# Kernel optimization log

Measured on AMD Instinct MI355X. Metric: run time of the kernel, lower is better.

Reference implementation:

```python
import jax, jax.numpy as jnp
import numpy as np

N = 100_000
E = 1_600_000
IN, HID, HEADS, OUT = 128, 64, 4, 64
LAYER_DIMS = [(IN, HEADS, HID // HEADS), (HID, HEADS, HID // HEADS), (HID, 1, OUT)]
NEG_SLOPE = 0.2


def setup_inputs() -> dict:
    key = jax.random.key(0)
    ks = jax.random.split(key, 20)
    inp = {}
    inp["x"] = jax.random.normal(ks[0], (N, IN), dtype=jnp.float32)
    # edges with src != dst by construction (module removes self loops, then adds them)
    for i in range(3):
        src = jax.random.randint(ks[1 + 2 * i], (E,), 0, N, dtype=jnp.int32)
        off = jax.random.randint(ks[2 + 2 * i], (E,), 1, N, dtype=jnp.int32)
        dst = ((src + off) % N).astype(jnp.int32)
        inp[f"edge_index{i}"] = jnp.stack([src, dst])
    k = 7
    for i, (cin, h, c) in enumerate(LAYER_DIMS):
        ws = 1.0 / np.sqrt(cin)
        inp[f"Wl{i}"] = jax.random.normal(ks[k], (cin, h * c), dtype=jnp.float32) * ws; k += 1
        inp[f"bl{i}"] = jnp.zeros((h * c,), dtype=jnp.float32)
        inp[f"Wr{i}"] = jax.random.normal(ks[k], (cin, h * c), dtype=jnp.float32) * ws; k += 1
        inp[f"br{i}"] = jnp.zeros((h * c,), dtype=jnp.float32)
        inp[f"att{i}"] = jax.random.normal(ks[k], (h, c), dtype=jnp.float32) * (1.0 / np.sqrt(c)); k += 1
        inp[f"bias{i}"] = jnp.zeros((h * c,), dtype=jnp.float32)
    return inp


def _l1norm(x):
    return x / jnp.maximum(jnp.sum(jnp.abs(x), axis=1, keepdims=True), 1e-12)


def _gat2conv(x, ei, Wl, bl, Wr, br, att, bias, heads, out_c):
    n = x.shape[0]
    xl = (x @ Wl + bl).reshape(n, heads, out_c)  # source-side features (x_j)
    xr = (x @ Wr + br).reshape(n, heads, out_c)  # target-side features (x_i)
    src, dst = ei[0], ei[1]
    s = jax.nn.leaky_relu(xl[src] + xr[dst], NEG_SLOPE)      # [E', H, C]
    a = jnp.einsum('ehc,hc->eh', s, att)                      # [E', H]
    m = jax.ops.segment_max(a, dst, num_segments=n)           # segment softmax over edges per target
    e = jnp.exp(a - m[dst])
    den = jax.ops.segment_sum(e, dst, num_segments=n)
    alpha = e / (den[dst] + 1e-16)
    msg = (xl[src] * alpha[:, :, None]).reshape(-1, heads * out_c)
    return jax.ops.segment_sum(msg, dst, num_segments=n) + bias  # concat heads + bias


def _forward(x, eis, params):
    loop = jnp.arange(N, dtype=eis[0].dtype)
    self_loops = jnp.stack([loop, loop])
    num_layers = len(LAYER_DIMS)
    for i, ((cin, h, c), p) in enumerate(zip(LAYER_DIMS, params)):
        ei = jnp.concatenate([eis[i], self_loops], axis=1)  # add_self_loops
        new_x = _gat2conv(x, ei, *p, h, c)
        x = new_x
        if i != num_layers - 1:
            x = jax.nn.relu(new_x)
        x = _l1norm(x)  # F.normalize(x, p=1)
    x = x / jnp.maximum(jnp.linalg.norm(x, axis=1, keepdims=True), 1e-12)  # F.normalize (L2)
    return jax.nn.relu(x)


def reference(x, edge_index0, edge_index1, edge_index2,
              Wl0, bl0, Wr0, br0, att0, bias0,
              Wl1, bl1, Wr1, br1, att1, bias1,
              Wl2, bl2, Wr2, br2, att2, bias2):
    eis = (edge_index0, edge_index1, edge_index2)
    params = [(Wl0, bl0, Wr0, br0, att0, bias0),
              (Wl1, bl1, Wr1, br1, att1, bias1),
              (Wl2, bl2, Wr2, br2, att2, bias2)]
    return _forward(x, eis, params)
```

## Files before the change

### kernel.cpp

```cpp
#include <hip/hip_runtime.h>
#include <hip/hip_fp16.h>
#include <string.h>

#define NN 100000
#define EE 1600000
#define CAP 64
#define NBIN 196
#define BINSZ 512
#define BINCAP 10400
#define CHA 2048
#define NCA 782
#define GGX 391

typedef __fp16 h2v __attribute__((ext_vector_type(2)));
typedef __fp16 half8 __attribute__((ext_vector_type(8)));
typedef float  f32x4 __attribute__((ext_vector_type(4)));

template<int CTRL>
__device__ __forceinline__ float dppadd(float x){
    int y = __builtin_amdgcn_update_dpp(0, __float_as_int(x), CTRL, 0xF, 0xF, true);
    return x + __int_as_float(y);
}
template<int H>
__device__ __forceinline__ float head_reduce32(float p){
    p = dppadd<0xB1>(p);
    p = dppadd<0x4E>(p);
    p = dppadd<0x141>(p);
    if constexpr (H == 1){
        p = dppadd<0x140>(p);
        p += __shfl_xor(p, 16);
    }
    return p;
}
__device__ __forceinline__ float red32(float p){
    p = dppadd<0xB1>(p);
    p = dppadd<0x4E>(p);
    p = dppadd<0x141>(p);
    p = dppadd<0x140>(p);
    p += __shfl_xor(p, 16);
    return p;
}


__global__ __launch_bounds__(256) void k_A(
    const int* __restrict__ e0, const int* __restrict__ e1, const int* __restrict__ e2,
    int* __restrict__ p0, int* __restrict__ p1, int* __restrict__ p2,
    int* __restrict__ tail)
{
    __shared__ int h4[4][NBIN];
    __shared__ int shist[NBIN], lbase[NBIN], gbase[NBIN], cur[NBIN];
    __shared__ int pk[CHA], spp[CHA];
    const int l = blockIdx.x / NCA, c = blockIdx.x % NCA;
    const int* ei = (l==0? e0 : l==1? e1 : e2);
    int* pr = (l==0? p0 : l==1? p1 : p2);
    const int base = c*CHA, n = min(CHA, EE-base);
    const int tid = threadIdx.x;
    const int wave = tid >> 6;
    for (int i=tid;i<4*NBIN;i+=256) ((int*)h4)[i]=0;
    __syncthreads();
    int dreg[CHA/256], sreg[CHA/256];
    #pragma unroll
    for (int j = 0; j < CHA/256; ++j){
        const int i = tid + j*256;
        if (i < n){ dreg[j] = ei[EE+base+i]; sreg[j] = ei[base+i]; }
        else { dreg[j] = -1; }
    }
    #pragma unroll
    for (int j = 0; j < CHA/256; ++j)
        if (dreg[j] >= 0) atomicAdd(&h4[wave][dreg[j]>>9],1);
    __syncthreads();
    for (int i=tid;i<NBIN;i+=256) shist[i] = h4[0][i]+h4[1][i]+h4[2][i]+h4[3][i];
    __syncthreads();
    if (tid==0){ int acc=0; for (int i=0;i<NBIN;++i){ lbase[i]=acc; acc+=shist[i]; } }
    __syncthreads();
    if (tid<NBIN){ gbase[tid] = atomicAdd(&tail[l*NBIN+tid], shist[tid]); cur[tid]=lbase[tid]; }
    __syncthreads();
    #pragma unroll
    for (int j = 0; j < CHA/256; ++j){
        if (dreg[j] < 0) continue;
        const int d = dreg[j], s = sreg[j];
        const int bb = d>>9;
        const int r = atomicAdd(&cur[bb],1);
        const int off = gbase[bb] + (r - lbase[bb]);
        pk[r] = (s << 9) | (d & 511);
        spp[r] = (off < BINCAP) ? (bb*BINCAP + off) : -1;
    }
    __syncthreads();
    for (int i=tid;i<n;i+=256){ const int p = spp[i]; if (p >= 0) pr[p] = pk[i]; }
}

__global__ __launch_bounds__(256) void k_B(
    const int* __restrict__ p0, const int* __restrict__ p1, const int* __restrict__ p2,
    const int* __restrict__ tail,
    int* __restrict__ c0, int* __restrict__ s0,
    int* __restrict__ c1, int* __restrict__ s1,
    int* __restrict__ c2, int* __restrict__ s2)
{
    __shared__ int cnt[BINSZ];
    __shared__ __align__(16) int sl[BINSZ*CAP];
    const int l = blockIdx.x / NBIN, b = blockIdx.x % NBIN;
    const int* pr = (l==0? p0 : l==1? p1 : p2) + (size_t)b*BINCAP;
    int* gc = (l==0? c0 : l==1? c1 : c2);
    int* gs = (l==0? s0 : l==1? s1 : s2);
    const int n0 = b*BINSZ;
    const int nn = min(BINSZ, NN - n0);
    const int tid = threadIdx.x;
    for (int i=tid;i<nn;i+=256){ cnt[i]=1; sl[i*CAP]= n0+i; }
    __syncthreads();
    const int ec = min(tail[l*NBIN+b], BINCAP);
    for (int i=tid;i<ec;i+=256){
        const int pv = pr[i];
        const int nd = pv & 511;
        const int p = atomicAdd(&cnt[nd],1);
        if (p < CAP) sl[nd*CAP+p] = pv >> 9;
    }
    __syncthreads();
    for (int i=tid;i<nn;i+=256) gc[n0+i] = cnt[i];
    const int t4 = nn*(CAP/4);
    int4* gs4 = (int4*)(gs + (size_t)n0*CAP);
    const int4* sl4 = (const int4*)sl;
    for (int i=tid;i<t4;i+=256) gs4[i] = sl4[i];
}


template<int CIN>
__global__ __launch_bounds__(256) void k_gemm(
    const float* __restrict__ x,
    const float* __restrict__ Wl, const float* __restrict__ bl,
    const float* __restrict__ Wr, const float* __restrict__ br,
    __half* __restrict__ xlh, float* __restrict__ xr)
{
    constexpr int KC = CIN / 32;
    const int tid = threadIdx.x;
    const int wave = tid >> 6, lane = tid & 63;
    const int m = lane & 15, g = lane >> 4;
    const int side = blockIdx.y;
    const float* __restrict__ W  = side ? Wr : Wl;
    const float* __restrict__ bb = side ? br : bl;

    half8 bf[4][KC];
    #pragma unroll
    for (int ct = 0; ct < 4; ++ct)
        #pragma unroll
        for (int kc = 0; kc < KC; ++kc)
            #pragma unroll
            for (int i = 0; i < 8; ++i)
                bf[ct][kc][i] = (__fp16)W[(kc*32 + g*8 + i)*64 + ct*16 + m];

    float bv[4];
    #pragma unroll
    for (int ct = 0; ct < 4; ++ct) bv[ct] = bb[ct*16 + m];

    const int stride = GGX * 64;
    for (int row0 = blockIdx.x*64 + wave*16; row0 < NN; row0 += stride){
        half8 a[KC];
        const float* xp = x + (size_t)(row0 + m) * CIN + g*8;
        #pragma unroll
        for (int kc = 0; kc < KC; ++kc){
            const float4 u = *(const float4*)(xp + kc*32);
            const float4 v = *(const float4*)(xp + kc*32 + 4);
            a[kc][0]=(__fp16)u.x; a[kc][1]=(__fp16)u.y; a[kc][2]=(__fp16)u.z; a[kc][3]=(__fp16)u.w;
            a[kc][4]=(__fp16)v.x; a[kc][5]=(__fp16)v.y; a[kc][6]=(__fp16)v.z; a[kc][7]=(__fp16)v.w;
        }
        f32x4 acc0 = {0,0,0,0}, acc1 = {0,0,0,0}, acc2 = {0,0,0,0}, acc3 = {0,0,0,0};
        #pragma unroll
        for (int kc = 0; kc < KC; ++kc){
            acc0 = __builtin_amdgcn_mfma_f32_16x16x32_f16(a[kc], bf[0][kc], acc0, 0,0,0);
            acc1 = __builtin_amdgcn_mfma_f32_16x16x32_f16(a[kc], bf[1][kc], acc1, 0,0,0);
            acc2 = __builtin_amdgcn_mfma_f32_16x16x32_f16(a[kc], bf[2][kc], acc2, 0,0,0);
            acc3 = __builtin_amdgcn_mfma_f32_16x16x32_f16(a[kc], bf[3][kc], acc3, 0,0,0);
        }
        #pragma unroll
        for (int j = 0; j < 4; ++j){
            const size_t rb = (size_t)(row0 + 4*g + j)*64 + m;
            const float o0 = acc0[j] + bv[0];
            const float o1 = acc1[j] + bv[1];
            const float o2 = acc2[j] + bv[2];
            const float o3 = acc3[j] + bv[3];
            if (side){
                xr[rb]    = o0; xr[rb+16] = o1; xr[rb+32] = o2; xr[rb+48] = o3;
            } else {
                xlh[rb]    = __float2half_rn(o0);
                xlh[rb+16] = __float2half_rn(o1);
                xlh[rb+32] = __float2half_rn(o2);
                xlh[rb+48] = __float2half_rn(o3);
            }
        }
    }
}

template<int H, bool LAST>
__global__ __launch_bounds__(256) void k_fused(
    const int* __restrict__ cnt, const int* __restrict__ slots,
    const __half* __restrict__ xlh, const float* __restrict__ xr,
    const float* __restrict__ att, const float* __restrict__ bias,
    float* __restrict__ out)
{
    const int lane = threadIdx.x & 63;
    const int hl = lane >> 5;
    const int c  = lane & 31;
    const int node = __builtin_amdgcn_readfirstlane(blockIdx.x * 4 + (threadIdx.x >> 6));
    if (node >= NN) return;

    const float2 xr2f = *(const float2*)(xr + (size_t)node*64 + 2*c);
    const h2v xr2 = { (__fp16)xr2f.x, (__fp16)xr2f.y };
    const float2 at2f = *(const float2*)(att + 2*c);
    const h2v at2 = { (__fp16)(at2f.x * 1.44269504088896f),
                      (__fp16)(at2f.y * 1.44269504088896f) };
    const float2 bias2 = *(const float2*)(bias + 2*c);
    const h2v k02 = { (__fp16)0.2f, (__fp16)0.2f };

    int deg = __builtin_amdgcn_readfirstlane(cnt[node]);
    deg = deg > CAP ? CAP : deg;
    const int dm1 = deg - 1;
    const int* __restrict__ sp = slots + (size_t)node * CAP;

    float den = 0.f, a0 = 0.f, a1 = 0.f;
    const int ngrp = (deg + 7) >> 3;

    for (int g = 0; g < ngrp; ++g){
        const int b0 = g*8;
        int ein[4]; h2v x2[4]; float q[4], e[4];
        #pragma unroll
        for (int j = 0; j < 4; ++j){
            ein[j] = b0 + 2*j + hl;
            const int ec = ein[j] < dm1 ? ein[j] : dm1;
            const int id = sp[ec];
            x2[j] = *(const h2v*)(xlh + (size_t)id*64 + 2*c);
        }
        #pragma unroll
        for (int j = 0; j < 4; ++j){
            h2v v = x2[j] + xr2;
            v = __builtin_elementwise_max(v, v * k02);
            q[j] = head_reduce32<H>(__builtin_amdgcn_fdot2(v, at2, 0.f, false));
        }
        if (b0 + 8 > deg){
            #pragma unroll
            for (int j = 0; j < 4; ++j) if (ein[j] > dm1) q[j] = -16384.f;
        }
        #pragma unroll
        for (int j = 0; j < 4; ++j) e[j] = __builtin_amdgcn_exp2f(q[j]);
        #pragma unroll
        for (int j = 0; j < 4; ++j){
            a0 = fmaf(e[j], (float)x2[j][0], a0);
            a1 = fmaf(e[j], (float)x2[j][1], a1);
        }
        den += (e[0]+e[1]) + (e[2]+e[3]);
    }
    a0 += __shfl_xor(a0, 32);
    a1 += __shfl_xor(a1, 32);
    den += __shfl_xor(den, 32);

    const float rd = __builtin_amdgcn_rcpf(den);
    float o0 = fmaf(a0, rd, bias2.x);
    float o1 = fmaf(a1, rd, bias2.y);
    if (!LAST){ o0 = fmaxf(o0, 0.f); o1 = fmaxf(o1, 0.f); }
    const float ns = red32(fabsf(o0) + fabsf(o1));
    const float rs = __builtin_amdgcn_rcpf(fmaxf(ns, 1e-12f));
    o0 *= rs; o1 *= rs;
    if (LAST){
        const float qq = red32(o0*o0 + o1*o1);
        const float rq = __builtin_amdgcn_rsqf(fmaxf(qq, 1e-24f));
        o0 = fmaxf(o0*rq, 0.f); o1 = fmaxf(o1*rq, 0.f);
    }
    if (hl == 0) *(float2*)(out + (size_t)node*64 + 2*c) = make_float2(o0, o1);
}

__global__ __launch_bounds__(256) void k_init(int* __restrict__ cnt, int* __restrict__ slots)
{
    const int i = blockIdx.x * 256 + threadIdx.x;
    if (i < NN){ cnt[i] = 1; slots[(size_t)i * CAP] = i; }
}
__global__ __launch_bounds__(256) void k_build(
    const int* __restrict__ ei, int* __restrict__ cnt, int* __restrict__ slots)
{
    const int stride = gridDim.x * 256;
    for (int e = blockIdx.x * 256 + threadIdx.x; e < EE; e += stride){
        const int s = ei[e], d = ei[e + EE];
        const int pos = atomicAdd(&cnt[d], 1);
        if (pos < CAP) slots[(size_t)d * CAP + pos] = s;
    }
}

extern "C" void kernel_launch(void* const* d_in, const int* in_sizes, int n_in,
                              void* d_out, int out_size, void* d_ws, size_t ws_size,
                              hipStream_t stream)
{
    const float* x0 = (const float*)d_in[0];
    const int* ei[3] = {(const int*)d_in[1], (const int*)d_in[2], (const int*)d_in[3]};
    const float *Wl[3], *bl[3], *Wr[3], *br[3], *att[3], *bias[3];
    for (int i = 0; i < 3; ++i){
        Wl[i]   = (const float*)d_in[4 + 6*i];
        bl[i]   = (const float*)d_in[5 + 6*i];
        Wr[i]   = (const float*)d_in[6 + 6*i];
        br[i]   = (const float*)d_in[7 + 6*i];
        att[i]  = (const float*)d_in[8 + 6*i];
        bias[i] = (const float*)d_in[9 + 6*i];
    }
    float* out = (float*)d_out;

    const size_t NN64 = (size_t)NN * 64;
    __half* xlh = (__half*)d_ws;
    float*  xr  = (float*)((char*)d_ws + NN64*2);
    float*  xb  = out;
    int* base = (int*)(xr + NN64);

    const size_t fused_need = NN64*2 + NN64*4 + (3*(size_t)NN*(CAP+1) + 3*NBIN)*4;

    dim3 blk(256);
    dim3 ggrid2(GGX, 2);
    const int ngrid = (NN + 3) / 4;
    const int igrid = (NN + 255) / 256;

    if (ws_size >= fused_need){
        int* c0 = base;                 int* s0 = c0 + NN;
        int* c1 = s0 + (size_t)NN*CAP;  int* s1 = c1 + NN;
        int* c2 = s1 + (size_t)NN*CAP;  int* s2 = c2 + NN;
        int* tail = s2 + (size_t)NN*CAP;
        int* p0 = (int*)out;
        int* p1 = (int*)d_ws;
        int* p2 = p1 + (size_t)NBIN*BINCAP;

        (void)hipMemsetAsync(tail, 0, 3*NBIN*sizeof(int), stream);
        k_A<<<3*NCA, blk, 0, stream>>>(ei[0], ei[1], ei[2], p0, p1, p2, tail);
        k_B<<<3*NBIN, blk, 0, stream>>>(p0, p1, p2, tail, c0, s0, c1, s1, c2, s2);

        k_gemm<128><<<ggrid2, blk, 0, stream>>>(x0, Wl[0], bl[0], Wr[0], br[0], xlh, xr);
        k_fused<4,false><<<ngrid, blk, 0, stream>>>(c0, s0, xlh, xr, att[0], bias[0], xb);
        k_gemm<64><<<ggrid2, blk, 0, stream>>>(xb, Wl[1], bl[1], Wr[1], br[1], xlh, xr);
        k_fused<4,false><<<ngrid, blk, 0, stream>>>(c1, s1, xlh, xr, att[1], bias[1], xb);
        k_gemm<64><<<ggrid2, blk, 0, stream>>>(xb, Wl[2], bl[2], Wr[2], br[2], xlh, xr);
        k_fused<1,true><<<ngrid, blk, 0, stream>>>(c2, s2, xlh, xr, att[2], bias[2], out);
    } else {
        int* cnt = base;
        int* slots = cnt + NN;

        k_init<<<igrid, blk, 0, stream>>>(cnt, slots);
        k_gemm<128><<<ggrid2, blk, 0, stream>>>(x0, Wl[0], bl[0], Wr[0], br[0], xlh, xr);
        k_build<<<512, blk, 0, stream>>>(ei[0], cnt, slots);
        k_fused<4,false><<<ngrid, blk, 0, stream>>>(cnt, slots, xlh, xr, att[0], bias[0], xb);

        k_init<<<igrid, blk, 0, stream>>>(cnt, slots);
        k_gemm<64><<<ggrid2, blk, 0, stream>>>(xb, Wl[1], bl[1], Wr[1], br[1], xlh, xr);
        k_build<<<512, blk, 0, stream>>>(ei[1], cnt, slots);
        k_fused<4,false><<<ngrid, blk, 0, stream>>>(cnt, slots, xlh, xr, att[1], bias[1], xb);

        k_init<<<igrid, blk, 0, stream>>>(cnt, slots);
        k_gemm<64><<<ggrid2, blk, 0, stream>>>(xb, Wl[2], bl[2], Wr[2], br[2], xlh, xr);
        k_build<<<512, blk, 0, stream>>>(ei[2], cnt, slots);
        k_fused<1,true><<<ngrid, blk, 0, stream>>>(cnt, slots, xlh, xr, att[2], bias[2], out);
    }
}
```

Measured before the change: 339.5 us.

## Process four edges per wave with 16 lanes per node row in GAT aggregation

The fused attention/aggregation kernel now gives each lane four channels instead of two. Each wave covers a 64-channel node row with 16 lanes and handles four edges at once in place of two. Gathers become 8-byte loads, head reductions become shorter DPP chains within 16 lanes, and the cross-lane shuffle at the end of the row reduction is removed. In exchange, the final accumulation needs two shuffle steps, and each lane holds more registers.

```diff
diff --git a/kernel.cpp b/kernel.cpp
--- a/kernel.cpp
+++ b/kernel.cpp
@@ -22,22 +22,20 @@
     return x + __int_as_float(y);
 }
 template<int H>
-__device__ __forceinline__ float head_reduce32(float p){
+__device__ __forceinline__ float head_reduce16(float p){
     p = dppadd<0xB1>(p);
     p = dppadd<0x4E>(p);
-    p = dppadd<0x141>(p);
     if constexpr (H == 1){
+        p = dppadd<0x141>(p);
         p = dppadd<0x140>(p);
-        p += __shfl_xor(p, 16);
     }
     return p;
 }
-__device__ __forceinline__ float red32(float p){
+__device__ __forceinline__ float red16(float p){
     p = dppadd<0xB1>(p);
     p = dppadd<0x4E>(p);
     p = dppadd<0x141>(p);
     p = dppadd<0x140>(p);
-    p += __shfl_xor(p, 16);
     return p;
 }
 
@@ -197,17 +195,19 @@
     float* __restrict__ out)
 {
     const int lane = threadIdx.x & 63;
-    const int hl = lane >> 5;
-    const int c  = lane & 31;
+    const int sub = lane >> 4;
+    const int c  = lane & 15;
     const int node = __builtin_amdgcn_readfirstlane(blockIdx.x * 4 + (threadIdx.x >> 6));
     if (node >= NN) return;
-
-    const float2 xr2f = *(const float2*)(xr + (size_t)node*64 + 2*c);
-    const h2v xr2 = { (__fp16)xr2f.x, (__fp16)xr2f.y };
-    const float2 at2f = *(const float2*)(att + 2*c);
-    const h2v at2 = { (__fp16)(at2f.x * 1.44269504088896f),
-                      (__fp16)(at2f.y * 1.44269504088896f) };
-    const float2 bias2 = *(const float2*)(bias + 2*c);
+    constexpr float L2E = 1.44269504088896f;
+
+    const float4 xr4 = *(const float4*)(xr + (size_t)node*64 + 4*c);
+    const h2v xra = { (__fp16)xr4.x, (__fp16)xr4.y };
+    const h2v xrb = { (__fp16)xr4.z, (__fp16)xr4.w };
+    const float4 at4 = *(const float4*)(att + 4*c);
+    const h2v ata = { (__fp16)(at4.x*L2E), (__fp16)(at4.y*L2E) };
+    const h2v atb = { (__fp16)(at4.z*L2E), (__fp16)(at4.w*L2E) };
+    const float4 b4 = *(const float4*)(bias + 4*c);
     const h2v k02 = { (__fp16)0.2f, (__fp16)0.2f };
 
     int deg = __builtin_amdgcn_readfirstlane(cnt[node]);
@@ -215,55 +215,53 @@
     const int dm1 = deg - 1;
     const int* __restrict__ sp = slots + (size_t)node * CAP;
 
-    float den = 0.f, a0 = 0.f, a1 = 0.f;
+    float den = 0.f, a0 = 0.f, a1 = 0.f, a2 = 0.f, a3 = 0.f;
     const int ngrp = (deg + 7) >> 3;
 
     for (int g = 0; g < ngrp; ++g){
         const int b0 = g*8;
-        int ein[4]; h2v x2[4]; float q[4], e[4];
-        #pragma unroll
-        for (int j = 0; j < 4; ++j){
-            ein[j] = b0 + 2*j + hl;
-            const int ec = ein[j] < dm1 ? ein[j] : dm1;
+        #pragma unroll
+        for (int jj = 0; jj < 2; ++jj){
+            const int eidx = b0 + 4*jj + sub;
+            const int ec = eidx < dm1 ? eidx : dm1;
             const int id = sp[ec];
-            x2[j] = *(const h2v*)(xlh + (size_t)id*64 + 2*c);
+            const uint2 u = *(const uint2*)(xlh + (size_t)id*64 + 4*c);
+            h2v xa, xb; memcpy(&xa, &u.x, 4); memcpy(&xb, &u.y, 4);
+            h2v va = xa + xra, vb = xb + xrb;
+            va = __builtin_elementwise_max(va, va * k02);
+            vb = __builtin_elementwise_max(vb, vb * k02);
+            float q = head_reduce16<H>(__builtin_amdgcn_fdot2(va, ata,
+                        __builtin_amdgcn_fdot2(vb, atb, 0.f, false), false));
+            q = (eidx <= dm1) ? q : -16384.f;
+            const float e = __builtin_amdgcn_exp2f(q);
+            a0 = fmaf(e, (float)xa[0], a0);
+            a1 = fmaf(e, (float)xa[1], a1);
+            a2 = fmaf(e, (float)xb[0], a2);
+            a3 = fmaf(e, (float)xb[1], a3);
+            den += e;
         }
-        #pragma unroll
-        for (int j = 0; j < 4; ++j){
-            h2v v = x2[j] + xr2;
-            v = __builtin_elementwise_max(v, v * k02);
-            q[j] = head_reduce32<H>(__builtin_amdgcn_fdot2(v, at2, 0.f, false));
-        }
-        if (b0 + 8 > deg){
-            #pragma unroll
-            for (int j = 0; j < 4; ++j) if (ein[j] > dm1) q[j] = -16384.f;
-        }
-        #pragma unroll
-        for (int j = 0; j < 4; ++j) e[j] = __builtin_amdgcn_exp2f(q[j]);
-        #pragma unroll
-        for (int j = 0; j < 4; ++j){
-            a0 = fmaf(e[j], (float)x2[j][0], a0);
-            a1 = fmaf(e[j], (float)x2[j][1], a1);
-        }
-        den += (e[0]+e[1]) + (e[2]+e[3]);
-    }
-    a0 += __shfl_xor(a0, 32);
-    a1 += __shfl_xor(a1, 32);
-    den += __shfl_xor(den, 32);
+    }
+    a0 += __shfl_xor(a0,16); a0 += __shfl_xor(a0,32);
+    a1 += __shfl_xor(a1,16); a1 += __shfl_xor(a1,32);
+    a2 += __shfl_xor(a2,16); a2 += __shfl_xor(a2,32);
+    a3 += __shfl_xor(a3,16); a3 += __shfl_xor(a3,32);
+    den += __shfl_xor(den,16); den += __shfl_xor(den,32);
 
     const float rd = __builtin_amdgcn_rcpf(den);
-    float o0 = fmaf(a0, rd, bias2.x);
-    float o1 = fmaf(a1, rd, bias2.y);
-    if (!LAST){ o0 = fmaxf(o0, 0.f); o1 = fmaxf(o1, 0.f); }
-    const float ns = red32(fabsf(o0) + fabsf(o1));
+    float o0 = fmaf(a0, rd, b4.x);
+    float o1 = fmaf(a1, rd, b4.y);
+    float o2 = fmaf(a2, rd, b4.z);
+    float o3 = fmaf(a3, rd, b4.w);
+    if (!LAST){ o0=fmaxf(o0,0.f); o1=fmaxf(o1,0.f); o2=fmaxf(o2,0.f); o3=fmaxf(o3,0.f); }
+    const float ns = red16((fabsf(o0)+fabsf(o1)) + (fabsf(o2)+fabsf(o3)));
     const float rs = __builtin_amdgcn_rcpf(fmaxf(ns, 1e-12f));
-    o0 *= rs; o1 *= rs;
+    o0 *= rs; o1 *= rs; o2 *= rs; o3 *= rs;
     if (LAST){
-        const float qq = red32(o0*o0 + o1*o1);
+        const float qq = red16((o0*o0+o1*o1) + (o2*o2+o3*o3));
         const float rq = __builtin_amdgcn_rsqf(fmaxf(qq, 1e-24f));
-        o0 = fmaxf(o0*rq, 0.f); o1 = fmaxf(o1*rq, 0.f);
-    }
-    if (hl == 0) *(float2*)(out + (size_t)node*64 + 2*c) = make_float2(o0, o1);
+        o0=fmaxf(o0*rq,0.f); o1=fmaxf(o1*rq,0.f); o2=fmaxf(o2*rq,0.f); o3=fmaxf(o3*rq,0.f);
+    }
+    if (sub == 0) *(float4*)(out + (size_t)node*64 + 4*c) = make_float4(o0,o1,o2,o3);
 }
 
 __global__ __launch_bounds__(256) void k_init(int* __restrict__ cnt, int* __restrict__ slots)
```

Measured after the change: 323.7 us. 1.05x faster.
